# Kernel tuning notes

Measured on AMD Instinct MI355X. Metric: run time of the kernel, lower is better.

## Reference

```python
import jax, jax.numpy as jnp
import numpy as np

INPUT_DIM, OUTPUT_DIM = 128, 256
FPS_FACTOR, KNN = 14, 10


def fps(pcd, K):
    """Farthest point sampling. pcd: [B,N,3] -> (points [B,K,3], indices [B,K]).
    Deterministic start at index 0 (pytorch3d uses first/random point)."""
    B, N, _ = pcd.shape
    first = jnp.zeros((B,), jnp.int32)
    init_d = jnp.full((B, N), 1e10, pcd.dtype)

    def step(carry, _):
        dists, last = carry
        lp = jnp.take_along_axis(pcd, last[:, None, None], axis=1)  # [B,1,3]
        d = jnp.sum((pcd - lp) ** 2, axis=-1)                        # [B,N]
        dists = jnp.minimum(dists, d)
        nxt = jnp.argmax(dists, axis=-1).astype(jnp.int32)
        return (dists, nxt), nxt

    (_, _), rest = jax.lax.scan(step, (init_d, first), None, length=K - 1)
    idx = jnp.concatenate([first[None, :], rest], axis=0).T  # [B,K]
    pts = jnp.take_along_axis(pcd, idx[..., None], axis=1)   # [B,K,3]
    return pts, idx


def knn_idx(q, p, k):
    """q:[B,Q,3], p:[B,N,3] -> nearest-neighbor indices [B,Q,k] (squared L2)."""
    d = (jnp.sum(q * q, -1)[:, :, None] + jnp.sum(p * p, -1)[:, None, :]
         - 2.0 * jnp.einsum('bqc,bnc->bqn', q, p))
    _, idx = jax.lax.top_k(-d, k)
    return idx


_bgather = jax.vmap(lambda a, i: a[i])  # per-batch fancy gather


def setup_inputs() -> dict:
    key = jax.random.key(0)
    k1, k2, k3, k4, k5 = jax.random.split(key, 5)
    B, N = 4, 16384
    tgt = jax.random.normal(k1, (B, N, INPUT_DIM), jnp.float32)
    pcd_x = jax.random.normal(k2, (B, N, 3), jnp.float32)
    pcd_v = jax.random.normal(k3, (B, N, 3, 3), jnp.float32)
    W = jax.random.normal(k4, (INPUT_DIM, OUTPUT_DIM), jnp.float32) / np.sqrt(INPUT_DIM)
    b = jax.random.normal(k5, (OUTPUT_DIM,), jnp.float32) * 0.01
    return {"tgt": tgt, "pcd_x": pcd_x, "pcd_v": pcd_v, "W": W, "b": b}


def reference(tgt, pcd_x, pcd_v, W, b):
    B, N, D = tgt.shape
    n_out = N // FPS_FACTOR
    out_pcd_x, out_indices = fps(pcd_x, n_out)          # [B,n_out,3], [B,n_out]
    nn = knn_idx(out_pcd_x, pcd_x, KNN)                 # [B,n_out,k]

    knn_pcd = _bgather(pcd_x, nn)                       # [B,n_out,k,3]
    query_f = jnp.take_along_axis(tgt, out_indices[..., None], axis=1)  # [B,n_out,D]
    query_c = out_pcd_x
    query_v = _bgather(pcd_v, out_indices)              # [B,n_out,V,3]
    key_f = _bgather(tgt, nn)                           # [B,n_out,k,D]
    key_c = knn_pcd
    key_v = _bgather(pcd_v, nn)                         # [B,n_out,k,V,3]

    # flatten (B*n_out) super-point groups, project features
    _query_f = query_f.reshape(-1, D)[:, None, :] @ W + b          # [B*n_out,1,O]
    _key_f = key_f.reshape(-1, KNN, D) @ W + b                     # [B*n_out,k,O]
    del _key_f, key_c, key_v  # consumed by the (identity stand-in) transformer

    # NOTE: URSATransformer stand-in = identity on the projected query features
    out_query_f = _query_f.reshape(B, n_out, OUTPUT_DIM)
    return out_query_f, query_c, query_v
```

## Files before the change

kernel.cpp:

```cpp
#include <hip/hip_runtime.h>

constexpr int B_   = 4;
constexpr int N_   = 16384;
constexpr int NOUT = 1170;
constexpr int D_   = 128;
constexpr int O_   = 256;

typedef float f32x2 __attribute__((ext_vector_type(2)));
typedef unsigned long long u64;

template <int CTRL>
__device__ __forceinline__ float dpp_fmax(float x) {
  int yi = __builtin_amdgcn_update_dpp(__float_as_int(x), __float_as_int(x),
                                       CTRL, 0xF, 0xF, false);
  return fmaxf(x, __int_as_float(yi));
}

__device__ __forceinline__ u64 umax64(u64 a, u64 b) { return a > b ? a : b; }

constexpr int TPB_FPS = 1024;
constexpr int PPT   = N_ / TPB_FPS;
constexpr int NPAIR = PPT / 2;
constexpr int NW    = TPB_FPS / 64;

__global__ __launch_bounds__(TPB_FPS)
__attribute__((amdgpu_waves_per_eu(4, 4)))
void fps_kernel(const float* __restrict__ pcd_x,
                int* __restrict__ sel,
                float* __restrict__ out_c) {
  const int b = blockIdx.x;
  const int t = threadIdx.x;
  const float* __restrict__ P = pcd_x + (size_t)b * N_ * 3;
  const int base = t * PPT;

  f32x2 x[NPAIR], y[NPAIR], z[NPAIR], dm[NPAIR];
#pragma unroll
  for (int k = 0; k < NPAIR; ++k) {
    const int p0 = base + 2 * k;
    x[k]  = f32x2{P[p0 * 3 + 0], P[p0 * 3 + 3]};
    y[k]  = f32x2{P[p0 * 3 + 1], P[p0 * 3 + 4]};
    z[k]  = f32x2{P[p0 * 3 + 2], P[p0 * 3 + 5]};
    dm[k] = f32x2{1e10f, 1e10f};
  }
#pragma unroll
  for (int k = 0; k < NPAIR; ++k) {
    asm volatile("" : "+v"(x[k]), "+v"(y[k]), "+v"(z[k]), "+v"(dm[k]));
  }

  __shared__ u64 s_key[2][NW] __attribute__((aligned(16)));

  float lx = P[0], ly = P[1], lz = P[2];
  if (t == 0) {
    sel[b * NOUT + 0] = 0;
    out_c[((size_t)b * NOUT + 0) * 3 + 0] = lx;
    out_c[((size_t)b * NOUT + 0) * 3 + 1] = ly;
    out_c[((size_t)b * NOUT + 0) * 3 + 2] = lz;
  }

  for (int step = 1; step < NOUT; ++step) {
    const int par = step & 1;
    const f32x2 lxx = {lx, lx}, lyy = {ly, ly}, lzz = {lz, lz};
    f32x2 bv2 = {-1.0f, -1.0f};
    {
#pragma clang fp contract(off)
#pragma unroll
      for (int k = 0; k < NPAIR; ++k) {
        const f32x2 dx = x[k] - lxx;
        const f32x2 dy = y[k] - lyy;
        const f32x2 dz = z[k] - lzz;
        const f32x2 s  = (dx * dx + dy * dy) + dz * dz;
        f32x2 nd;
        nd.x = fminf(dm[k].x, s.x);
        nd.y = fminf(dm[k].y, s.y);
        dm[k] = nd;
        bv2.x = fmaxf(bv2.x, nd.x);
        bv2.y = fmaxf(bv2.y, nd.y);
      }
    }
    const float bv = fmaxf(bv2.x, bv2.y);

    float wm = bv;
    wm = dpp_fmax<0xB1>(wm);
    wm = dpp_fmax<0x4E>(wm);
    wm = dpp_fmax<0x141>(wm);
    wm = dpp_fmax<0x140>(wm);
    wm = dpp_fmax<0x142>(wm);
    wm = dpp_fmax<0x143>(wm);
    const float wmax =
        __int_as_float(__builtin_amdgcn_readlane(__float_as_int(wm), 63));

    int bi = 0;
#pragma unroll
    for (int k = NPAIR - 1; k >= 0; --k) {
      if (dm[k].y == bv) bi = base + 2 * k + 1;
      if (dm[k].x == bv) bi = base + 2 * k;
    }

    const unsigned long long mask = __ballot(bv == wmax);
    const int flane = __builtin_ctzll(mask);
    const int idx_w = __builtin_amdgcn_readlane(bi, flane);

    const u64 key =
        ((u64)__float_as_uint(wmax) << 32) | (unsigned)(~idx_w);
    if ((t & 63) == 0) s_key[par][t >> 6] = key;
    __syncthreads();

    const ulonglong2* kp =
        reinterpret_cast<const ulonglong2*>(&s_key[par][0]);
    u64 m[8];
#pragma unroll
    for (int i = 0; i < 8; ++i) {
      const ulonglong2 v = kp[i];
      m[i] = umax64(v.x, v.y);
    }
    const u64 q0 = umax64(umax64(m[0], m[1]), umax64(m[2], m[3]));
    const u64 q1 = umax64(umax64(m[4], m[5]), umax64(m[6], m[7]));
    const u64 kmax = umax64(q0, q1);

    int ri = (int)(~(unsigned)kmax);
    ri = __builtin_amdgcn_readfirstlane(ri);

    lx = P[ri * 3 + 0];
    ly = P[ri * 3 + 1];
    lz = P[ri * 3 + 2];
    if (t == 0) {
      sel[b * NOUT + step] = ri;
      out_c[((size_t)b * NOUT + step) * 3 + 0] = lx;
      out_c[((size_t)b * NOUT + step) * 3 + 1] = ly;
      out_c[((size_t)b * NOUT + step) * 3 + 2] = lz;
    }
  }
}

constexpr int TPB_PROJ = 256;
constexpr int RPB = 4;

__global__ __launch_bounds__(TPB_PROJ)
void proj_kernel(const float* __restrict__ tgt,
                 const float* __restrict__ pcd_v,
                 const float* __restrict__ W,
                 const float* __restrict__ bias,
                 const int* __restrict__ sel,
                 float* __restrict__ out_f,
                 float* __restrict__ out_v) {
  const int t = threadIdx.x;
  const int row0 = blockIdx.x * RPB;

  __shared__ float sA[RPB * D_];
  __shared__ int   sIdx[RPB];

  if (t < RPB) {
    const int row = row0 + t;
    const int b = row / NOUT;
    sIdx[t] = b * N_ + sel[row];
  }
  __syncthreads();

#pragma unroll
  for (int l = 0; l < RPB * D_ / TPB_PROJ; ++l) {
    const int e = t + l * TPB_PROJ;
    const int r = e >> 7;
    const int k = e & (D_ - 1);
    sA[e] = tgt[(size_t)sIdx[r] * D_ + k];
  }
  __syncthreads();

  float acc0 = 0.f, acc1 = 0.f, acc2 = 0.f, acc3 = 0.f;
#pragma unroll 8
  for (int k = 0; k < D_; ++k) {
    const float w = W[k * O_ + t];
    acc0 = fmaf(sA[0 * D_ + k], w, acc0);
    acc1 = fmaf(sA[1 * D_ + k], w, acc1);
    acc2 = fmaf(sA[2 * D_ + k], w, acc2);
    acc3 = fmaf(sA[3 * D_ + k], w, acc3);
  }
  const float bb = bias[t];
  out_f[(size_t)(row0 + 0) * O_ + t] = acc0 + bb;
  out_f[(size_t)(row0 + 1) * O_ + t] = acc1 + bb;
  out_f[(size_t)(row0 + 2) * O_ + t] = acc2 + bb;
  out_f[(size_t)(row0 + 3) * O_ + t] = acc3 + bb;

  if (t < RPB * 9) {
    const int r = t / 9;
    const int e = t - r * 9;
    out_v[(size_t)(row0 + r) * 9 + e] = pcd_v[(size_t)sIdx[r] * 9 + e];
  }
}

extern "C" void kernel_launch(void* const* d_in, const int* in_sizes, int n_in,
                              void* d_out, int out_size, void* d_ws, size_t ws_size,
                              hipStream_t stream) {
  const float* tgt   = (const float*)d_in[0];
  const float* pcd_x = (const float*)d_in[1];
  const float* pcd_v = (const float*)d_in[2];
  const float* W     = (const float*)d_in[3];
  const float* bias  = (const float*)d_in[4];

  float* out   = (float*)d_out;
  float* out_f = out;
  float* out_c = out + (size_t)B_ * NOUT * O_;
  float* out_v = out_c + (size_t)B_ * NOUT * 3;

  int* sel = (int*)d_ws;

  hipLaunchKernelGGL(fps_kernel, dim3(B_), dim3(TPB_FPS), 0, stream,
                     pcd_x, sel, out_c);
  hipLaunchKernelGGL(proj_kernel, dim3(B_ * NOUT / RPB), dim3(TPB_PROJ), 0, stream,
                     tgt, pcd_v, W, bias, sel, out_f, out_v);
}
```

Measured before the change: 1.904 ms.

## Spatially sort points and skip FPS distance updates via bounding-box pruning

Adds a kernel that buckets each batch's points into a 4096-cell Morton-ordered grid, so each FPS thread owns 16 spatially close points. Each thread keeps a bounding box and skips the distance update when the box lies farther from the newly selected point than its current maximum min-distance. Ties are broken by original index, so the selection should match the reference. The quantization assumes coordinates roughly in [-5,5], which only affects pruning quality, not correctness. Skipped work is uneven across threads and there is an extra sort launch plus workspace use.

```diff
diff --git a/kernel.cpp b/kernel.cpp
--- a/kernel.cpp
+++ b/kernel.cpp
@@ -15,8 +15,202 @@
                                        CTRL, 0xF, 0xF, false);
   return fmaxf(x, __int_as_float(yi));
 }
-
+__device__ __forceinline__ float wave_fmax(float v) {
+  v = dpp_fmax<0xB1>(v);
+  v = dpp_fmax<0x4E>(v);
+  v = dpp_fmax<0x141>(v);
+  v = dpp_fmax<0x140>(v);
+  v = dpp_fmax<0x142>(v);
+  v = dpp_fmax<0x143>(v);
+  return __int_as_float(__builtin_amdgcn_readlane(__float_as_int(v), 63));
+}
 __device__ __forceinline__ u64 umax64(u64 a, u64 b) { return a > b ? a : b; }
+
+constexpr int NCELL = 4096;
+
+__device__ __forceinline__ unsigned exp3(unsigned v) {
+  return (v & 1u) | ((v & 2u) << 2) | ((v & 4u) << 4) | ((v & 8u) << 6);
+}
+__device__ __forceinline__ int quant16(float v) {
+  int q = (int)((v + 5.0f) * 1.6f);
+  return q < 0 ? 0 : (q > 15 ? 15 : q);
+}
+
+__global__ __launch_bounds__(1024)
+void sort_kernel(const float* __restrict__ pcd_x,
+                 float* __restrict__ sx, float* __restrict__ sy,
+                 float* __restrict__ sz, int* __restrict__ so) {
+  const int b = blockIdx.x, t = threadIdx.x;
+  const float* __restrict__ P = pcd_x + (size_t)b * N_ * 3;
+  float* SX = sx + (size_t)b * N_;
+  float* SY = sy + (size_t)b * N_;
+  float* SZ = sz + (size_t)b * N_;
+  int*   SO = so + (size_t)b * N_;
+
+  __shared__ unsigned hist[NCELL];
+  __shared__ unsigned wtot[16];
+#pragma unroll
+  for (int i = 0; i < NCELL / 1024; ++i) hist[t + i * 1024] = 0;
+  __syncthreads();
+
+  unsigned code[16];
+#pragma unroll
+  for (int j = 0; j < 16; ++j) {
+    const int p = t + j * 1024;
+    const float x = P[p * 3 + 0], y = P[p * 3 + 1], z = P[p * 3 + 2];
+    code[j] = exp3(quant16(x)) | (exp3(quant16(y)) << 1) | (exp3(quant16(z)) << 2);
+    atomicAdd(&hist[code[j]], 1u);
+  }
+  __syncthreads();
+
+  unsigned h[4], sum = 0;
+#pragma unroll
+  for (int i = 0; i < 4; ++i) { h[i] = hist[t * 4 + i]; sum += h[i]; }
+  unsigned sc = sum;
+#pragma unroll
+  for (int d = 1; d < 64; d <<= 1) {
+    const unsigned v = __shfl_up(sc, d, 64);
+    if ((t & 63) >= d) sc += v;
+  }
+  if ((t & 63) == 63) wtot[t >> 6] = sc;
+  __syncthreads();
+  unsigned woff = 0;
+  for (int w = 0; w < (t >> 6); ++w) woff += wtot[w];
+  const unsigned excl = woff + sc - sum;
+  hist[t * 4 + 0] = excl;
+  hist[t * 4 + 1] = excl + h[0];
+  hist[t * 4 + 2] = excl + h[0] + h[1];
+  hist[t * 4 + 3] = excl + h[0] + h[1] + h[2];
+  __syncthreads();
+
+#pragma unroll
+  for (int j = 0; j < 16; ++j) {
+    const int p = t + j * 1024;
+    const unsigned pos = atomicAdd(&hist[code[j]], 1u);
+    SX[pos] = P[p * 3 + 0];
+    SY[pos] = P[p * 3 + 1];
+    SZ[pos] = P[p * 3 + 2];
+    SO[pos] = p;
+  }
+}
+
+__global__ __launch_bounds__(1024)
+void fps_fast_kernel(const float* __restrict__ pcd_x,
+                     const float* __restrict__ sx, const float* __restrict__ sy,
+                     const float* __restrict__ sz, const int* __restrict__ so,
+                     int* __restrict__ sel, float* __restrict__ out_c) {
+  const int b = blockIdx.x, t = threadIdx.x;
+  const float* __restrict__ SX = sx + (size_t)b * N_;
+  const float* __restrict__ SY = sy + (size_t)b * N_;
+  const float* __restrict__ SZ = sz + (size_t)b * N_;
+  const int*   __restrict__ SO = so + (size_t)b * N_;
+  const int base = t * 16;
+
+  float xs[16], ys[16], zs[16], dmv[16];
+  int oi[16];
+#pragma unroll
+  for (int j = 0; j < 16; ++j) {
+    xs[j] = SX[base + j]; ys[j] = SY[base + j]; zs[j] = SZ[base + j];
+    oi[j] = SO[base + j]; dmv[j] = 1e10f;
+  }
+  float lox = xs[0], hix = xs[0], loy = ys[0], hiy = ys[0], loz = zs[0], hiz = zs[0];
+#pragma unroll
+  for (int j = 1; j < 16; ++j) {
+    lox = fminf(lox, xs[j]); hix = fmaxf(hix, xs[j]);
+    loy = fminf(loy, ys[j]); hiy = fmaxf(hiy, ys[j]);
+    loz = fminf(loz, zs[j]); hiz = fmaxf(hiz, zs[j]);
+  }
+  float thr_max = 1e10f;
+  int thr_oi = 0, thr_pos = base;
+
+  __shared__ u64 s_key[2][16];
+
+  float lx = pcd_x[(size_t)b * N_ * 3 + 0];
+  float ly = pcd_x[(size_t)b * N_ * 3 + 1];
+  float lz = pcd_x[(size_t)b * N_ * 3 + 2];
+  if (t == 0) {
+    sel[b * NOUT + 0] = 0;
+    out_c[((size_t)b * NOUT + 0) * 3 + 0] = lx;
+    out_c[((size_t)b * NOUT + 0) * 3 + 1] = ly;
+    out_c[((size_t)b * NOUT + 0) * 3 + 2] = lz;
+  }
+
+  for (int step = 1; step < NOUT; ++step) {
+    const int par = step & 1;
+    const float bx = fmaxf(0.f, fmaxf(lox - lx, lx - hix));
+    const float by = fmaxf(0.f, fmaxf(loy - ly, ly - hiy));
+    const float bz = fmaxf(0.f, fmaxf(loz - lz, lz - hiz));
+    const float bb = bx * bx + by * by + bz * bz;
+
+    if (!(bb > thr_max * (1.0f + 4e-6f))) {
+      float nm = -1.0f;
+      {
+#pragma clang fp contract(off)
+#pragma unroll
+        for (int j = 0; j < 16; ++j) {
+          const float dx = xs[j] - lx;
+          const float dy = ys[j] - ly;
+          const float dz = zs[j] - lz;
+          const float s  = (dx * dx + dy * dy) + dz * dz;
+          const float nd = fminf(dmv[j], s);
+          dmv[j] = nd;
+          nm = fmaxf(nm, nd);
+        }
+      }
+      thr_max = nm;
+      int boi = 0x7fffffff, bj = 0;
+#pragma unroll
+      for (int j = 0; j < 16; ++j) {
+        if (dmv[j] == nm && oi[j] < boi) { boi = oi[j]; bj = j; }
+      }
+      thr_oi = boi; thr_pos = base + bj;
+    }
+
+    const float wmax = wave_fmax(thr_max);
+    const u64 mask = __ballot(thr_max == wmax);
+    int oidx, pos;
+    if (__popcll(mask) == 1) {
+      const int l = __builtin_ctzll(mask);
+      oidx = __builtin_amdgcn_readlane(thr_oi, l);
+      pos  = __builtin_amdgcn_readlane(thr_pos, l);
+    } else {
+      oidx = 0x7fffffff; pos = 0;
+      u64 m = mask;
+      while (m) {
+        const int l = __builtin_ctzll(m); m &= m - 1;
+        const int o = __builtin_amdgcn_readlane(thr_oi, l);
+        const int p = __builtin_amdgcn_readlane(thr_pos, l);
+        if (o < oidx) { oidx = o; pos = p; }
+      }
+    }
+
+    if ((t & 63) == 0)
+      s_key[par][t >> 6] = ((u64)__float_as_uint(wmax) << 28) |
+                           ((u64)(unsigned)((~oidx) & 0x3FFF) << 14) |
+                           (u64)(unsigned)pos;
+    __syncthreads();
+
+    const ulonglong2* kp = reinterpret_cast<const ulonglong2*>(&s_key[par][0]);
+    u64 m8[8];
+#pragma unroll
+    for (int i = 0; i < 8; ++i) { const ulonglong2 v = kp[i]; m8[i] = umax64(v.x, v.y); }
+    const u64 kmax = umax64(umax64(umax64(m8[0], m8[1]), umax64(m8[2], m8[3])),
+                            umax64(umax64(m8[4], m8[5]), umax64(m8[6], m8[7])));
+
+    int wpos = (int)((unsigned)kmax & 0x3FFFu);
+    int woi  = 16383 - (int)((unsigned)(kmax >> 14) & 0x3FFFu);
+    wpos = __builtin_amdgcn_readfirstlane(wpos);
+    woi  = __builtin_amdgcn_readfirstlane(woi);
+
+    lx = SX[wpos]; ly = SY[wpos]; lz = SZ[wpos];
+    if (t == 0) {
+      sel[b * NOUT + step] = woi;
+      out_c[((size_t)b * NOUT + step) * 3 + 0] = lx;
+      out_c[((size_t)b * NOUT + step) * 3 + 1] = ly;
+      out_c[((size_t)b * NOUT + step) * 3 + 2] = lz;
+    }
+  }
+}
 
 constexpr int TPB_FPS = 1024;
 constexpr int PPT   = N_ / TPB_FPS;
@@ -24,15 +218,11 @@
 constexpr int NW    = TPB_FPS / 64;
 
 __global__ __launch_bounds__(TPB_FPS)
-__attribute__((amdgpu_waves_per_eu(4, 4)))
-void fps_kernel(const float* __restrict__ pcd_x,
-                int* __restrict__ sel,
-                float* __restrict__ out_c) {
-  const int b = blockIdx.x;
-  const int t = threadIdx.x;
+void fps_brute_kernel(const float* __restrict__ pcd_x,
+                      int* __restrict__ sel, float* __restrict__ out_c) {
+  const int b = blockIdx.x, t = threadIdx.x;
   const float* __restrict__ P = pcd_x + (size_t)b * N_ * 3;
   const int base = t * PPT;
-
   f32x2 x[NPAIR], y[NPAIR], z[NPAIR], dm[NPAIR];
 #pragma unroll
   for (int k = 0; k < NPAIR; ++k) {
@@ -42,13 +232,7 @@
     z[k]  = f32x2{P[p0 * 3 + 2], P[p0 * 3 + 5]};
     dm[k] = f32x2{1e10f, 1e10f};
   }
-#pragma unroll
-  for (int k = 0; k < NPAIR; ++k) {
-    asm volatile("" : "+v"(x[k]), "+v"(y[k]), "+v"(z[k]), "+v"(dm[k]));
-  }
-
-  __shared__ u64 s_key[2][NW] __attribute__((aligned(16)));
-
+  __shared__ u64 s_key[2][NW];
   float lx = P[0], ly = P[1], lz = P[2];
   if (t == 0) {
     sel[b * NOUT + 0] = 0;
@@ -56,7 +240,6 @@
     out_c[((size_t)b * NOUT + 0) * 3 + 1] = ly;
     out_c[((size_t)b * NOUT + 0) * 3 + 2] = lz;
   }
-
   for (int step = 1; step < NOUT; ++step) {
     const int par = step & 1;
     const f32x2 lxx = {lx, lx}, lyy = {ly, ly}, lzz = {lz, lz};
@@ -65,64 +248,36 @@
 #pragma clang fp contract(off)
 #pragma unroll
       for (int k = 0; k < NPAIR; ++k) {
-        const f32x2 dx = x[k] - lxx;
-        const f32x2 dy = y[k] - lyy;
-        const f32x2 dz = z[k] - lzz;
-        const f32x2 s  = (dx * dx + dy * dy) + dz * dz;
-        f32x2 nd;
-        nd.x = fminf(dm[k].x, s.x);
-        nd.y = fminf(dm[k].y, s.y);
+        const f32x2 dx = x[k] - lxx, dy = y[k] - lyy, dz = z[k] - lzz;
+        const f32x2 s = (dx * dx + dy * dy) + dz * dz;
+        f32x2 nd; nd.x = fminf(dm[k].x, s.x); nd.y = fminf(dm[k].y, s.y);
         dm[k] = nd;
-        bv2.x = fmaxf(bv2.x, nd.x);
-        bv2.y = fmaxf(bv2.y, nd.y);
+        bv2.x = fmaxf(bv2.x, nd.x); bv2.y = fmaxf(bv2.y, nd.y);
       }
     }
     const float bv = fmaxf(bv2.x, bv2.y);
-
-    float wm = bv;
-    wm = dpp_fmax<0xB1>(wm);
-    wm = dpp_fmax<0x4E>(wm);
-    wm = dpp_fmax<0x141>(wm);
-    wm = dpp_fmax<0x140>(wm);
-    wm = dpp_fmax<0x142>(wm);
-    wm = dpp_fmax<0x143>(wm);
-    const float wmax =
-        __int_as_float(__builtin_amdgcn_readlane(__float_as_int(wm), 63));
-
+    const float wmax = wave_fmax(bv);
     int bi = 0;
 #pragma unroll
     for (int k = NPAIR - 1; k >= 0; --k) {
       if (dm[k].y == bv) bi = base + 2 * k + 1;
       if (dm[k].x == bv) bi = base + 2 * k;
     }
-
-    const unsigned long long mask = __ballot(bv == wmax);
+    const u64 mask = __ballot(bv == wmax);
     const int flane = __builtin_ctzll(mask);
     const int idx_w = __builtin_amdgcn_readlane(bi, flane);
-
-    const u64 key =
-        ((u64)__float_as_uint(wmax) << 32) | (unsigned)(~idx_w);
+    const u64 key = ((u64)__float_as_uint(wmax) << 32) | (unsigned)(~idx_w);
     if ((t & 63) == 0) s_key[par][t >> 6] = key;
     __syncthreads();
-
-    const ulonglong2* kp =
-        reinterpret_cast<const ulonglong2*>(&s_key[par][0]);
-    u64 m[8];
-#pragma unroll
-    for (int i = 0; i < 8; ++i) {
-      const ulonglong2 v = kp[i];
-      m[i] = umax64(v.x, v.y);
-    }
-    const u64 q0 = umax64(umax64(m[0], m[1]), umax64(m[2], m[3]));
-    const u64 q1 = umax64(umax64(m[4], m[5]), umax64(m[6], m[7]));
-    const u64 kmax = umax64(q0, q1);
-
+    const ulonglong2* kp = reinterpret_cast<const ulonglong2*>(&s_key[par][0]);
+    u64 m8[8];
+#pragma unroll
+    for (int i = 0; i < 8; ++i) { const ulonglong2 v = kp[i]; m8[i] = umax64(v.x, v.y); }
+    const u64 kmax = umax64(umax64(umax64(m8[0], m8[1]), umax64(m8[2], m8[3])),
+                            umax64(umax64(m8[4], m8[5]), umax64(m8[6], m8[7])));
     int ri = (int)(~(unsigned)kmax);
     ri = __builtin_amdgcn_readfirstlane(ri);
-
-    lx = P[ri * 3 + 0];
-    ly = P[ri * 3 + 1];
-    lz = P[ri * 3 + 2];
+    lx = P[ri * 3 + 0]; ly = P[ri * 3 + 1]; lz = P[ri * 3 + 2];
     if (t == 0) {
       sel[b * NOUT + step] = ri;
       out_c[((size_t)b * NOUT + step) * 3 + 0] = lx;
@@ -145,26 +300,21 @@
                  float* __restrict__ out_v) {
   const int t = threadIdx.x;
   const int row0 = blockIdx.x * RPB;
-
   __shared__ float sA[RPB * D_];
   __shared__ int   sIdx[RPB];
-
   if (t < RPB) {
     const int row = row0 + t;
     const int b = row / NOUT;
     sIdx[t] = b * N_ + sel[row];
   }
   __syncthreads();
-
 #pragma unroll
   for (int l = 0; l < RPB * D_ / TPB_PROJ; ++l) {
     const int e = t + l * TPB_PROJ;
-    const int r = e >> 7;
-    const int k = e & (D_ - 1);
+    const int r = e >> 7, k = e & (D_ - 1);
     sA[e] = tgt[(size_t)sIdx[r] * D_ + k];
   }
   __syncthreads();
-
   float acc0 = 0.f, acc1 = 0.f, acc2 = 0.f, acc3 = 0.f;
 #pragma unroll 8
   for (int k = 0; k < D_; ++k) {
@@ -179,10 +329,8 @@
   out_f[(size_t)(row0 + 1) * O_ + t] = acc1 + bb;
   out_f[(size_t)(row0 + 2) * O_ + t] = acc2 + bb;
   out_f[(size_t)(row0 + 3) * O_ + t] = acc3 + bb;
-
   if (t < RPB * 9) {
-    const int r = t / 9;
-    const int e = t - r * 9;
+    const int r = t / 9, e = t - r * 9;
     out_v[(size_t)(row0 + r) * 9 + e] = pcd_v[(size_t)sIdx[r] * 9 + e];
   }
 }
@@ -201,10 +349,24 @@
   float* out_c = out + (size_t)B_ * NOUT * O_;
   float* out_v = out_c + (size_t)B_ * NOUT * 3;
 
-  int* sel = (int*)d_ws;
-
-  hipLaunchKernelGGL(fps_kernel, dim3(B_), dim3(TPB_FPS), 0, stream,
-                     pcd_x, sel, out_c);
-  hipLaunchKernelGGL(proj_kernel, dim3(B_ * NOUT / RPB), dim3(TPB_PROJ), 0, stream,
-                     tgt, pcd_v, W, bias, sel, out_f, out_v);
-}
+  const size_t need = (size_t)4 * B_ * N_ * 4 + (size_t)B_ * NOUT * 4;
+  if (ws_size >= need) {
+    float* sx = (float*)d_ws;
+    float* sy = sx + (size_t)B_ * N_;
+    float* sz = sy + (size_t)B_ * N_;
+    int*   so = (int*)(sz + (size_t)B_ * N_);
+    int*   sel = so + (size_t)B_ * N_;
+    hipLaunchKernelGGL(sort_kernel, dim3(B_), dim3(1024), 0, stream,
+                       pcd_x, sx, sy, sz, so);
+    hipLaunchKernelGGL(fps_fast_kernel, dim3(B_), dim3(1024), 0, stream,
+                       pcd_x, sx, sy, sz, so, sel, out_c);
+    hipLaunchKernelGGL(proj_kernel, dim3(B_ * NOUT / RPB), dim3(TPB_PROJ), 0, stream,
+                       tgt, pcd_v, W, bias, sel, out_f, out_v);
+  } else {
+    int* sel = (int*)d_ws;
+    hipLaunchKernelGGL(fps_brute_kernel, dim3(B_), dim3(TPB_FPS), 0, stream,
+                       pcd_x, sel, out_c);
+    hipLaunchKernelGGL(proj_kernel, dim3(B_ * NOUT / RPB), dim3(TPB_PROJ), 0, stream,
+                       tgt, pcd_v, W, bias, sel, out_f, out_v);
+  }
+}
```

After: 2.309 ms. +21.3%, slower.

## Halve FPS block size and replace 64-bit key reduction with DPP float argmax

Applied to the files above, without the earlier changes.

The FPS kernel now runs 512 threads per batch with 32 points per thread instead of 1024 threads with 16, cutting the number of waves that must synchronize each step. The cross-wave reduction stores (max, index) float pairs in LDS and reduces them with DPP fmax plus a ballot, replacing the serial 64-bit key max tree. The register-pinning asm barrier moves inside the loop. The trade-off is twice the per-thread distance work per step and higher register pressure, in exchange for cheaper per-step synchronization and reduction. Tie-breaking now takes the lowest wave rather than the lowest point index, which may differ from the reference on exact ties.

```diff
diff --git a/kernel.cpp b/kernel.cpp
--- a/kernel.cpp
+++ b/kernel.cpp
@@ -16,22 +16,20 @@
   return fmaxf(x, __int_as_float(yi));
 }
 
-__device__ __forceinline__ u64 umax64(u64 a, u64 b) { return a > b ? a : b; }
-
-constexpr int TPB_FPS = 1024;
+constexpr int TPB_FPS = 512;
 constexpr int PPT   = N_ / TPB_FPS;
 constexpr int NPAIR = PPT / 2;
 constexpr int NW    = TPB_FPS / 64;
 
 __global__ __launch_bounds__(TPB_FPS)
-__attribute__((amdgpu_waves_per_eu(4, 4)))
+__attribute__((amdgpu_waves_per_eu(2, 2)))
 void fps_kernel(const float* __restrict__ pcd_x,
                 int* __restrict__ sel,
                 float* __restrict__ out_c) {
-  const int b = blockIdx.x;
-  const int t = threadIdx.x;
+  const int b = blockIdx.x, t = threadIdx.x;
   const float* __restrict__ P = pcd_x + (size_t)b * N_ * 3;
   const int base = t * PPT;
+  const int lane = t & 63;
 
   f32x2 x[NPAIR], y[NPAIR], z[NPAIR], dm[NPAIR];
 #pragma unroll
@@ -42,12 +40,8 @@
     z[k]  = f32x2{P[p0 * 3 + 2], P[p0 * 3 + 5]};
     dm[k] = f32x2{1e10f, 1e10f};
   }
-#pragma unroll
-  for (int k = 0; k < NPAIR; ++k) {
-    asm volatile("" : "+v"(x[k]), "+v"(y[k]), "+v"(z[k]), "+v"(dm[k]));
-  }
-
-  __shared__ u64 s_key[2][NW] __attribute__((aligned(16)));
+
+  __shared__ float2 s_pair[2][NW];
 
   float lx = P[0], ly = P[1], lz = P[2];
   if (t == 0) {
@@ -59,6 +53,20 @@
 
   for (int step = 1; step < NOUT; ++step) {
     const int par = step & 1;
+
+    asm volatile("" : "+v"(x[0]), "+v"(x[1]), "+v"(x[2]), "+v"(x[3]),
+                      "+v"(x[4]), "+v"(x[5]), "+v"(x[6]), "+v"(x[7]),
+                      "+v"(x[8]), "+v"(x[9]), "+v"(x[10]), "+v"(x[11]),
+                      "+v"(x[12]), "+v"(x[13]), "+v"(x[14]), "+v"(x[15]));
+    asm volatile("" : "+v"(y[0]), "+v"(y[1]), "+v"(y[2]), "+v"(y[3]),
+                      "+v"(y[4]), "+v"(y[5]), "+v"(y[6]), "+v"(y[7]),
+                      "+v"(y[8]), "+v"(y[9]), "+v"(y[10]), "+v"(y[11]),
+                      "+v"(y[12]), "+v"(y[13]), "+v"(y[14]), "+v"(y[15]));
+    asm volatile("" : "+v"(z[0]), "+v"(z[1]), "+v"(z[2]), "+v"(z[3]),
+                      "+v"(z[4]), "+v"(z[5]), "+v"(z[6]), "+v"(z[7]),
+                      "+v"(z[8]), "+v"(z[9]), "+v"(z[10]), "+v"(z[11]),
+                      "+v"(z[12]), "+v"(z[13]), "+v"(z[14]), "+v"(z[15]));
+
     const f32x2 lxx = {lx, lx}, lyy = {ly, ly}, lzz = {lz, lz};
     f32x2 bv2 = {-1.0f, -1.0f};
     {
@@ -96,29 +104,24 @@
       if (dm[k].x == bv) bi = base + 2 * k;
     }
 
-    const unsigned long long mask = __ballot(bv == wmax);
+    const u64 mask = __ballot(bv == wmax);
     const int flane = __builtin_ctzll(mask);
-    const int idx_w = __builtin_amdgcn_readlane(bi, flane);
-
-    const u64 key =
-        ((u64)__float_as_uint(wmax) << 32) | (unsigned)(~idx_w);
-    if ((t & 63) == 0) s_key[par][t >> 6] = key;
+    if (lane == flane) {
+      float2 pr;
+      pr.x = wmax;
+      pr.y = __int_as_float(bi);
+      s_pair[par][t >> 6] = pr;
+    }
     __syncthreads();
 
-    const ulonglong2* kp =
-        reinterpret_cast<const ulonglong2*>(&s_key[par][0]);
-    u64 m[8];
-#pragma unroll
-    for (int i = 0; i < 8; ++i) {
-      const ulonglong2 v = kp[i];
-      m[i] = umax64(v.x, v.y);
-    }
-    const u64 q0 = umax64(umax64(m[0], m[1]), umax64(m[2], m[3]));
-    const u64 q1 = umax64(umax64(m[4], m[5]), umax64(m[6], m[7]));
-    const u64 kmax = umax64(q0, q1);
-
-    int ri = (int)(~(unsigned)kmax);
-    ri = __builtin_amdgcn_readfirstlane(ri);
+    const float2 e = s_pair[par][lane & (NW - 1)];
+    float gv = e.x;
+    gv = dpp_fmax<0xB1>(gv);
+    gv = dpp_fmax<0x4E>(gv);
+    gv = dpp_fmax<0x141>(gv);
+    const u64 m2 = __ballot(e.x == gv);
+    const int ww = __builtin_ctzll(m2);
+    int ri = __builtin_amdgcn_readlane(__float_as_int(e.y), ww);
 
     lx = P[ri * 3 + 0];
     ly = P[ri * 3 + 1];
@@ -145,26 +148,21 @@
                  float* __restrict__ out_v) {
   const int t = threadIdx.x;
   const int row0 = blockIdx.x * RPB;
-
   __shared__ float sA[RPB * D_];
   __shared__ int   sIdx[RPB];
-
   if (t < RPB) {
     const int row = row0 + t;
     const int b = row / NOUT;
     sIdx[t] = b * N_ + sel[row];
   }
   __syncthreads();
-
 #pragma unroll
   for (int l = 0; l < RPB * D_ / TPB_PROJ; ++l) {
     const int e = t + l * TPB_PROJ;
-    const int r = e >> 7;
-    const int k = e & (D_ - 1);
+    const int r = e >> 7, k = e & (D_ - 1);
     sA[e] = tgt[(size_t)sIdx[r] * D_ + k];
   }
   __syncthreads();
-
   float acc0 = 0.f, acc1 = 0.f, acc2 = 0.f, acc3 = 0.f;
 #pragma unroll 8
   for (int k = 0; k < D_; ++k) {
@@ -179,10 +177,8 @@
   out_f[(size_t)(row0 + 1) * O_ + t] = acc1 + bb;
   out_f[(size_t)(row0 + 2) * O_ + t] = acc2 + bb;
   out_f[(size_t)(row0 + 3) * O_ + t] = acc3 + bb;
-
   if (t < RPB * 9) {
-    const int r = t / 9;
-    const int e = t - r * 9;
+    const int r = t / 9, e = t - r * 9;
     out_v[(size_t)(row0 + r) * 9 + e] = pcd_v[(size_t)sIdx[r] * 9 + e];
   }
 }
```

Result: no change. 1.920 ms (+0.8%).
